# Kernel tuning notes

Measured on AMD Instinct MI355X. Metric: run time of the kernel, lower is better.

Reference implementation:

```python
import jax, jax.numpy as jnp
import numpy as np

B, N, C = 8, 8192, 512
H, DH = 8, C // 8
SCALE = 0.02


def setup_inputs() -> dict:
    key = jax.random.key(0)
    k0, k1, k2, k3, k4 = jax.random.split(key, 5)
    return {
        "x": jax.random.normal(k0, (B, N, C), dtype=jnp.float32),
        "w1": SCALE * jax.random.normal(k1, (2, H, DH, DH), dtype=jnp.float32),
        "b1": SCALE * jax.random.normal(k2, (2, H, DH), dtype=jnp.float32),
        "w2": SCALE * jax.random.normal(k3, (2, H, DH, DH), dtype=jnp.float32),
        "b2": SCALE * jax.random.normal(k4, (2, H, DH), dtype=jnp.float32),
    }


def reference(x, w1, b1, w2, b2):
    dtype = x.dtype
    x = x.astype(jnp.float32)
    b, n, c = x.shape
    xf = jnp.fft.rfft(x, axis=1, norm="ortho")            # [B, N//2+1, C] complex
    xf = xf.reshape(b, n // 2 + 1, H, DH)                  # [B, F, H, DH]
    xr, xi = jnp.real(xf), jnp.imag(xf)
    # per-head complex linear 1 + GELU (complex mult split into real/imag)
    o1r = jax.nn.gelu(
        jnp.einsum("bfhi,hio->bfho", xr, w1[0])
        - jnp.einsum("bfhi,hio->bfho", xi, w1[1]) + b1[0], approximate=False)
    o1i = jax.nn.gelu(
        jnp.einsum("bfhi,hio->bfho", xi, w1[0])
        + jnp.einsum("bfhi,hio->bfho", xr, w1[1]) + b1[1], approximate=False)
    # per-head complex linear 2
    o2r = (jnp.einsum("bfhi,hio->bfho", o1r, w2[0])
           - jnp.einsum("bfhi,hio->bfho", o1i, w2[1]) + b2[0])
    o2i = (jnp.einsum("bfhi,hio->bfho", o1i, w2[0])
           + jnp.einsum("bfhi,hio->bfho", o1r, w2[1]) + b2[1])
    yf = (o2r + 1j * o2i).reshape(b, n // 2 + 1, c)
    y = jnp.fft.irfft(yf, n=n, axis=1, norm="ortho")
    return y.astype(dtype)
```

## Files before the change

### kernel.cpp

```cpp
#include <hip/hip_runtime.h>
#include <math.h>

#define BB    8
#define NLEN  8192
#define CC    512
#define HH    8
#define DH    64
#define MH    4096
#define FREQ  4097
#define FP    4160
#define NSEQ  (BB*CC)
#define BHSZ  (65*4096)

#define KADDR(k) ((((k) >> 6) << 12) + ((k) & 63))

#define REGION_BYTES ((size_t)NSEQ * FP * 4ull)

static __device__ __align__(256) unsigned char g_scratch[2ull * (size_t)NSEQ * FP * 4ull];
__device__ unsigned short g_wprep[8 * 4 * 64 * 64];

typedef __attribute__((ext_vector_type(8))) short bf16x8;
typedef __attribute__((ext_vector_type(4))) float f32x4;
typedef __attribute__((ext_vector_type(4))) unsigned u32x4;

__device__ __forceinline__ f32x4 MFMA(bf16x8 a, bf16x8 b, f32x4 c){
  return __builtin_amdgcn_mfma_f32_16x16x32_bf16(a, b, c, 0, 0, 0);
}

__device__ __forceinline__ unsigned short f2bf(float f){
  unsigned u = __float_as_uint(f);
  return (unsigned short)((u + 0x7fffu + ((u >> 16) & 1u)) >> 16);
}
__device__ __forceinline__ unsigned pack2(float a, float b){
  return (unsigned)f2bf(a) | ((unsigned)f2bf(b) << 16);
}
__device__ __forceinline__ float bflo(unsigned u){ return __uint_as_float(u << 16); }
__device__ __forceinline__ float bfhi(unsigned u){ return __uint_as_float(u & 0xffff0000u); }

__device__ const float C32C[16] = {
  1.f, 0.98078528f, 0.92387953f, 0.83146961f, 0.70710678f, 0.55557023f,
  0.38268343f, 0.19509032f, 0.f, -0.19509032f, -0.38268343f, -0.55557023f,
  -0.70710678f, -0.83146961f, -0.92387953f, -0.98078528f};
__device__ const float C32S[16] = {
  0.f, 0.19509032f, 0.38268343f, 0.55557023f, 0.70710678f, 0.83146961f,
  0.92387953f, 0.98078528f, 1.f, 0.98078528f, 0.92387953f, 0.83146961f,
  0.70710678f, 0.55557023f, 0.38268343f, 0.19509032f};

__device__ __forceinline__ float gelu_fast(float v){
  float x  = v * 0.70710678118654752440f;
  float ax = fabsf(x);
  float t  = __builtin_amdgcn_rcpf(fmaf(0.3275911f, ax, 1.0f));
  float p  = fmaf(fmaf(fmaf(fmaf(1.061405429f, t, -1.453152027f), t,
                            1.421413741f), t, -0.284496736f), t, 0.254829592f);
  float e  = __expf(-x * x);
  float erf_ax = fmaf(-p * t, e, 1.0f);
  float erfx = copysignf(erf_ax, x);
  return 0.5f * v * (1.0f + erfx);
}

__device__ __forceinline__ float2 cadd(float2 a, float2 b){ return make_float2(a.x+b.x, a.y+b.y); }
__device__ __forceinline__ float2 csub(float2 a, float2 b){ return make_float2(a.x-b.x, a.y-b.y); }
__device__ __forceinline__ float2 cmul(float2 a, float2 b){
  return make_float2(fmaf(a.x, b.x, -(a.y*b.y)), fmaf(a.x, b.y, a.y*b.x));
}

__global__ __launch_bounds__(256) void transpose_in_k(const float* __restrict__ in,
                                                      unsigned* __restrict__ out){
  __shared__ float tile[64][33];
  int b  = blockIdx.z;
  int c0 = blockIdx.x * 32;
  int n0 = blockIdx.y * 64;
  int t  = threadIdx.x;
  int tx = t & 31, ty = t >> 5;
  const float* src = in + ((size_t)b * NLEN + n0) * CC + c0;
  #pragma unroll
  for (int k = 0; k < 8; ++k)
    tile[ty + 8*k][tx] = src[(size_t)(ty + 8*k) * CC + tx];
  __syncthreads();
  int lt = t & 15;
  int nl = 4 * lt;
  #pragma unroll
  for (int kk = 0; kk < 2; ++kk){
    int cl = (t >> 4) + 16*kk;
    uint2 u;
    u.x = pack2(tile[nl    ][cl], tile[nl + 1][cl]);
    u.y = pack2(tile[nl + 2][cl], tile[nl + 3][cl]);
    *(uint2*)(out + ((size_t)(b * CC + c0 + cl) * NLEN + n0) / 2 + 2*lt) = u;
  }
}

__global__ __launch_bounds__(256) void transpose_out_k(const unsigned* __restrict__ in,
                                                       float* __restrict__ out){
  __shared__ float tile[64][33];
  int b  = blockIdx.z;
  int c0 = blockIdx.x * 32;
  int n0 = blockIdx.y * 64;
  int t  = threadIdx.x;
  int lt = t & 15;
  int nl = 4 * lt;
  #pragma unroll
  for (int kk = 0; kk < 2; ++kk){
    int cl = (t >> 4) + 16*kk;
    uint2 u = *(const uint2*)(in + ((size_t)(b * CC + c0 + cl) * NLEN + n0) / 2 + 2*lt);
    tile[nl    ][cl] = bflo(u.x);
    tile[nl + 1][cl] = bfhi(u.x);
    tile[nl + 2][cl] = bflo(u.y);
    tile[nl + 3][cl] = bfhi(u.y);
  }
  __syncthreads();
  int tx = t & 31, ty = t >> 5;
  float* dst = out + ((size_t)b * NLEN + n0) * CC + c0;
  #pragma unroll
  for (int k = 0; k < 8; ++k)
    dst[(size_t)(ty + 8*k) * CC + tx] = tile[ty + 8*k][tx];
}

#define SL(e) ((e) + ((e) >> 4))
#define PERM16(p) ((((p) & 3) << 2) | ((p) >> 2))

template<int SIGN>
__device__ __forceinline__ void dft4ip(float2& v0, float2& v1, float2& v2, float2& v3){
  float2 s02 = cadd(v0, v2), d02 = csub(v0, v2);
  float2 s13 = cadd(v1, v3), d13 = csub(v1, v3);
  float2 id = make_float2(-(float)SIGN * d13.y, (float)SIGN * d13.x);
  v0 = cadd(s02, s13);
  v1 = cadd(d02, id);
  v2 = csub(s02, s13);
  v3 = csub(d02, id);
}

template<int SIGN>
__device__ __forceinline__ float2 w16c(int m){
  const float c1 = 0.9238795325112867f, s1 = 0.3826834323650898f, r = 0.7071067811865476f;
  float cs = 1.f, sn = 0.f;
  if (m == 1){ cs = c1;  sn = s1; }
  else if (m == 2){ cs = r;   sn = r; }
  else if (m == 3){ cs = s1;  sn = c1; }
  else if (m == 4){ cs = 0.f; sn = 1.f; }
  else if (m == 6){ cs = -r;  sn = r; }
  else if (m == 9){ cs = -c1; sn = -s1; }
  return make_float2(cs, (float)SIGN * sn);
}

template<int SIGN>
__device__ __forceinline__ void dft16ip(float2 v[16]){
  #pragma unroll
  for (int q0 = 0; q0 < 4; ++q0) dft4ip<SIGN>(v[q0], v[q0+4], v[q0+8], v[q0+12]);
  #pragma unroll
  for (int p0 = 0; p0 < 4; ++p0)
    #pragma unroll
    for (int q0 = 0; q0 < 4; ++q0){
      const int m = p0 * q0;
      if (m) v[q0 + 4*p0] = cmul(v[q0 + 4*p0], w16c<SIGN>(m));
    }
  #pragma unroll
  for (int p0 = 0; p0 < 4; ++p0) dft4ip<SIGN>(v[4*p0], v[4*p0+1], v[4*p0+2], v[4*p0+3]);
}

template<int SIGN>
__device__ __forceinline__ void twiddle16(float2 v[16], int jm, float invRNs){
  float ang = (float)SIGN * 6.2831853071795864769f * (float)jm * invRNs;
  float sn, cs; __sincosf(ang, &sn, &cs);
  float2 tw[16];
  tw[1] = make_float2(cs, sn);
  #pragma unroll
  for (int q = 2; q < 16; ++q) tw[q] = cmul(tw[q >> 1], tw[q - (q >> 1)]);
  #pragma unroll
  for (int q = 1; q < 16; ++q) v[q] = cmul(v[q], tw[q]);
}

template<int SIGN, int NS>
__device__ __forceinline__ void fft_mid_pass(float2* lds2, float2 v[16], int t){
  #pragma unroll
  for (int q = 0; q < 16; ++q) v[q] = lds2[SL(t + 256*q)];
  int jm = t & (NS - 1);
  if (NS > 1) twiddle16<SIGN>(v, jm, 1.0f / (16.0f * (float)NS));
  dft16ip<SIGN>(v);
  __syncthreads();
  int base = ((t - jm) << 4) + jm;
  #pragma unroll
  for (int p = 0; p < 16; ++p) lds2[SL(base + p*NS)] = v[PERM16(p)];
  __syncthreads();
}

#define ORTHO_S 0.011048543456039806f

__global__ __launch_bounds__(256) void fft_fwd_k(const unsigned* __restrict__ xt,
                                                 unsigned* __restrict__ spec){
  __shared__ float2 lds2[4352];
  int t = threadIdx.x;
  size_t row = blockIdx.x;
  const unsigned* src = xt + row * (NLEN/2);
  float2 v[16];
  #pragma unroll
  for (int q = 0; q < 16; ++q){
    unsigned u = src[t + 256*q];
    v[q] = make_float2(bflo(u), bfhi(u));
  }
  dft16ip<-1>(v);
  #pragma unroll
  for (int p = 0; p < 16; ++p) lds2[SL(16*t + p)] = v[PERM16(p)];
  __syncthreads();
  fft_mid_pass<-1, 16 >(lds2, v, t);
  fft_mid_pass<-1, 256>(lds2, v, t);
  unsigned* dst = spec + (row >> 6) * (size_t)BHSZ + (row & 63) * 64;
  float snb, csb;
  __sincosf(-6.2831853071795864769f * (float)t / (float)NLEN, &snb, &csb);
  #pragma unroll
  for (int q = 0; q < 8; ++q){
    int k = t + 256*q;
    float2 zk = lds2[SL(k)];
    float2 zc = lds2[SL((MH - k) & (MH - 1))];
    float ex = 0.5f*(zk.x + zc.x);
    float ey = 0.5f*(zk.y - zc.y);
    float ox =  0.5f*(zk.y + zc.y);
    float oy = -0.5f*(zk.x - zc.x);
    float cs = fmaf(csb, C32C[q],  snb*C32S[q]);
    float sn = fmaf(snb, C32C[q], -csb*C32S[q]);
    float P = cs*ox - sn*oy;
    float Q = cs*oy + sn*ox;
    dst[KADDR(k)]      = pack2(ORTHO_S*(ex + P), ORTHO_S*(ey + Q));
    dst[KADDR(MH - k)] = pack2(ORTHO_S*(ex - P), ORTHO_S*(Q - ey));
  }
  if (t == 0){
    float2 zm = lds2[SL(2048)];
    dst[KADDR(2048)] = pack2(ORTHO_S*zm.x, -ORTHO_S*zm.y);
  }
}

__global__ __launch_bounds__(256) void fft_inv_k(const unsigned* __restrict__ spec,
                                                 unsigned* __restrict__ yt){
  __shared__ float2 lds2[4352];
  int t = threadIdx.x;
  size_t row = blockIdx.x;
  const unsigned* src = spec + (row >> 6) * (size_t)BHSZ + (row & 63) * 64;
  float snb, csb;
  __sincosf(6.2831853071795864769f * (float)t / (float)NLEN, &snb, &csb);
  #pragma unroll
  for (int q = 0; q < 8; ++q){
    int k = t + 256*q;
    unsigned uk = src[KADDR(k)];
    unsigned uc = src[KADDR(MH - k)];
    float2 xk = make_float2(bflo(uk), bfhi(uk));
    float2 xc = make_float2(bflo(uc), bfhi(uc));
    if (k == 0){ xk.y = 0.0f; xc.y = 0.0f; }
    float ex = xk.x + xc.x;
    float ey = xk.y - xc.y;
    float dx = xk.x - xc.x;
    float dy = xk.y + xc.y;
    float cs = fmaf(csb, C32C[q], -snb*C32S[q]);
    float sn = fmaf(snb, C32C[q],  csb*C32S[q]);
    float ox = cs*dx - sn*dy;
    float oy = cs*dy + sn*dx;
    lds2[SL(k)] = make_float2(ex - oy, ey + ox);
    if (k > 0)
      lds2[SL(MH - k)] = make_float2(ex + oy, ox - ey);
  }
  if (t == 0){
    unsigned um = src[KADDR(2048)];
    lds2[SL(2048)] = make_float2(2.0f*bflo(um), -2.0f*bfhi(um));
  }
  __syncthreads();
  float2 v[16];
  fft_mid_pass<1, 1  >(lds2, v, t);
  fft_mid_pass<1, 16 >(lds2, v, t);
  fft_mid_pass<1, 256>(lds2, v, t);
  uint4* d4 = (uint4*)(yt + row * (NLEN/2) + 16*t);
  #pragma unroll
  for (int g = 0; g < 4; ++g){
    float2 w0 = lds2[SL(16*t + 4*g    )];
    float2 w1 = lds2[SL(16*t + 4*g + 1)];
    float2 w2 = lds2[SL(16*t + 4*g + 2)];
    float2 w3 = lds2[SL(16*t + 4*g + 3)];
    uint4 stv;
    stv.x = pack2(ORTHO_S*w0.x, ORTHO_S*w0.y);
    stv.y = pack2(ORTHO_S*w1.x, ORTHO_S*w1.y);
    stv.z = pack2(ORTHO_S*w2.x, ORTHO_S*w2.y);
    stv.w = pack2(ORTHO_S*w3.x, ORTHO_S*w3.y);
    d4[g] = stv;
  }
}

__global__ __launch_bounds__(256) void wprep_k(const float* __restrict__ w1,
                                               const float* __restrict__ w2){
  int t = threadIdx.x;
  int h = blockIdx.x;
  #pragma unroll 4
  for (int u = 0; u < 64; ++u){
    int idx = t + 256*u;
    int p = idx >> 12;
    int o = (idx >> 6) & 63;
    int jj = idx & 63;
    int swo = (o ^ (o >> 3)) & 7;
    int s = (((jj >> 3) ^ swo) << 3) | (jj & 7);
    int i;
    if (p < 2){
      i = s;
    } else {
      int ks = s >> 5, g = (s >> 3) & 3, j = s & 7;
      i = (2*ks + (j >> 2))*16 + 4*g + (j & 3);
    }
    const float* src = (p < 2) ? w1 : w2;
    float v = src[(size_t)(p & 1) * 32768 + (size_t)h * 4096 + i * 64 + o];
    g_wprep[(size_t)h * 16384 + idx] = f2bf(v);
  }
}

__global__ __launch_bounds__(256) void afno_mid_mfma_k(const unsigned* __restrict__ spec_in,
                                                       unsigned* __restrict__ spec_out,
                                                       const float* __restrict__ b1,
                                                       const float* __restrict__ b2){
  __shared__ unsigned short Wl[16384];
  const int t = threadIdx.x;
  const int bx = blockIdx.x, h = blockIdx.y, b = blockIdx.z;
  const size_t bhoff = (size_t)(b * HH + h) * BHSZ + (size_t)bx * 4096;
  const int l = t & 63, wv = t >> 6;
  const int lf = l & 15, lg = l >> 4;
  const int wf0 = wv * 16;

  const unsigned* xblk = spec_in + bhoff;
  unsigned bins[16];
  #pragma unroll
  for (int ks = 0; ks < 2; ++ks){
    int i0 = (ks*4 + lg) * 8;
    #pragma unroll
    for (int j = 0; j < 8; ++j)
      bins[ks*8 + j] = xblk[(i0 + j)*64 + wf0 + lf];
  }

  {
    const uint4* gw  = (const uint4*)(g_wprep + (size_t)h * 16384);
    uint4*       sw4 = (uint4*)Wl;
    #pragma unroll
    for (int u = 0; u < 8; ++u) sw4[t + 256*u] = gw[t + 256*u];
  }
  float4 br1[4], bi1[4];
  #pragma unroll
  for (int mt = 0; mt < 4; ++mt){
    br1[mt] = *(const float4*)(b1 +       (size_t)h*64 + mt*16 + lg*4);
    bi1[mt] = *(const float4*)(b1 + 512 + (size_t)h*64 + mt*16 + lg*4);
  }
  float b2r[4], b2i[4];
  #pragma unroll
  for (int nt = 0; nt < 4; ++nt){
    b2r[nt] = b2[(size_t)h*64 + nt*16 + lf];
    b2i[nt] = b2[512 + (size_t)h*64 + nt*16 + lf];
  }
  __syncthreads();

  const unsigned short* W1R = Wl;
  const unsigned short* W1I = Wl + 4096;
  const unsigned short* W2R = Wl + 8192;
  const unsigned short* W2I = Wl + 12288;
  const f32x4 zz = {0.f, 0.f, 0.f, 0.f};

  f32x4 a1R[4], a1I[4];
  #pragma unroll
  for (int mt = 0; mt < 4; ++mt){ a1R[mt] = zz; a1I[mt] = zz; }

  #pragma unroll
  for (int ks = 0; ks < 2; ++ks){
    u32x4 pr, pi;
    pr.x = __builtin_amdgcn_perm(bins[ks*8+1], bins[ks*8+0], 0x05040100u);
    pr.y = __builtin_amdgcn_perm(bins[ks*8+3], bins[ks*8+2], 0x05040100u);
    pr.z = __builtin_amdgcn_perm(bins[ks*8+5], bins[ks*8+4], 0x05040100u);
    pr.w = __builtin_amdgcn_perm(bins[ks*8+7], bins[ks*8+6], 0x05040100u);
    pi.x = __builtin_amdgcn_perm(bins[ks*8+1], bins[ks*8+0], 0x07060302u);
    pi.y = __builtin_amdgcn_perm(bins[ks*8+3], bins[ks*8+2], 0x07060302u);
    pi.z = __builtin_amdgcn_perm(bins[ks*8+5], bins[ks*8+4], 0x07060302u);
    pi.w = __builtin_amdgcn_perm(bins[ks*8+7], bins[ks*8+6], 0x07060302u);
    bf16x8 bxr = __builtin_bit_cast(bf16x8, pr);
    bf16x8 bxi = __builtin_bit_cast(bf16x8, pi);
    int b0 = ks*4 + lg;
    #pragma unroll
    for (int mt = 0; mt < 4; ++mt){
      int o = mt*16 + lf;
      int swo = (o ^ (o >> 3)) & 7;
      int off = o*64 + ((b0 ^ swo) << 3);
      bf16x8 awr  = *(const bf16x8*)(W1R + off);
      bf16x8 awi  = *(const bf16x8*)(W1I + off);
      bf16x8 awin = awi ^ (short)0x8000;
      a1R[mt] = MFMA(awr,  bxr, a1R[mt]);
      a1R[mt] = MFMA(awin, bxi, a1R[mt]);
      a1I[mt] = MFMA(awi,  bxr, a1I[mt]);
      a1I[mt] = MFMA(awr,  bxi, a1I[mt]);
    }
  }

  bf16x8 aFr[2], aFi[2], aFin[2];
  #pragma unroll
  for (int ks = 0; ks < 2; ++ks){
    const int m0 = 2*ks, m1 = 2*ks + 1;
    u32x4 wr4, wi4;
    wr4.x = pack2(gelu_fast(a1R[m0][0] + br1[m0].x), gelu_fast(a1R[m0][1] + br1[m0].y));
    wr4.y = pack2(gelu_fast(a1R[m0][2] + br1[m0].z), gelu_fast(a1R[m0][3] + br1[m0].w));
    wr4.z = pack2(gelu_fast(a1R[m1][0] + br1[m1].x), gelu_fast(a1R[m1][1] + br1[m1].y));
    wr4.w = pack2(gelu_fast(a1R[m1][2] + br1[m1].z), gelu_fast(a1R[m1][3] + br1[m1].w));
    wi4.x = pack2(gelu_fast(a1I[m0][0] + bi1[m0].x), gelu_fast(a1I[m0][1] + bi1[m0].y));
    wi4.y = pack2(gelu_fast(a1I[m0][2] + bi1[m0].z), gelu_fast(a1I[m0][3] + bi1[m0].w));
    wi4.z = pack2(gelu_fast(a1I[m1][0] + bi1[m1].x), gelu_fast(a1I[m1][1] + bi1[m1].y));
    wi4.w = pack2(gelu_fast(a1I[m1][2] + bi1[m1].z), gelu_fast(a1I[m1][3] + bi1[m1].w));
    aFr[ks]  = __builtin_bit_cast(bf16x8, wr4);
    aFi[ks]  = __builtin_bit_cast(bf16x8, wi4);
    aFin[ks] = aFi[ks] ^ (short)0x8000;
  }

  f32x4 a2R[4], a2I[4];
  #pragma unroll
  for (int nt = 0; nt < 4; ++nt){ a2R[nt] = zz; a2I[nt] = zz; }
  #pragma unroll
  for (int ks = 0; ks < 2; ++ks){
    int b0 = ks*4 + lg;
    #pragma unroll
    for (int nt = 0; nt < 4; ++nt){
      int o2 = nt*16 + lf;
      int swo = (o2 ^ (o2 >> 3)) & 7;
      int off = o2*64 + ((b0 ^ swo) << 3);
      bf16x8 bwr = *(const bf16x8*)(W2R + off);
      bf16x8 bwi = *(const bf16x8*)(W2I + off);
      a2R[nt] = MFMA(aFr[ks],  bwr, a2R[nt]);
      a2R[nt] = MFMA(aFin[ks], bwi, a2R[nt]);
      a2I[nt] = MFMA(aFi[ks],  bwr, a2I[nt]);
      a2I[nt] = MFMA(aFr[ks],  bwi, a2I[nt]);
    }
  }

  unsigned* oblk = spec_out + bhoff;
  int fl0 = wf0 + lg*4;
  #pragma unroll
  for (int nt = 0; nt < 4; ++nt){
    int o2 = nt*16 + lf;
    uint4 st;
    st.x = pack2(a2R[nt][0] + b2r[nt], a2I[nt][0] + b2i[nt]);
    st.y = pack2(a2R[nt][1] + b2r[nt], a2I[nt][1] + b2i[nt]);
    st.z = pack2(a2R[nt][2] + b2r[nt], a2I[nt][2] + b2i[nt]);
    st.w = pack2(a2R[nt][3] + b2r[nt], a2I[nt][3] + b2i[nt]);
    *(uint4*)(oblk + o2*64 + fl0) = st;
  }
}

extern "C" void kernel_launch(void* const* d_in, const int* in_sizes, int n_in,
                              void* d_out, int out_size, void* d_ws, size_t ws_size,
                              hipStream_t stream) {
  const float* x  = (const float*)d_in[0];
  const float* w1 = (const float*)d_in[1];
  const float* b1 = (const float*)d_in[2];
  const float* w2 = (const float*)d_in[3];
  const float* b2 = (const float*)d_in[4];
  float* out = (float*)d_out;

  unsigned char* base = (unsigned char*)d_ws;
  if (ws_size < 2 * REGION_BYTES){
    void* p = nullptr;
    hipGetSymbolAddress(&p, HIP_SYMBOL(g_scratch));
    base = (unsigned char*)p;
  }
  unsigned* specA = (unsigned*)base;
  unsigned char* regB = base + REGION_BYTES;
  unsigned* xt    = (unsigned*)regB;
  unsigned* specB = (unsigned*)regB;
  unsigned* ytp   = (unsigned*)base;

  wprep_k<<<8, 256, 0, stream>>>(w1, w2);
  transpose_in_k<<<dim3(CC/32, NLEN/64, BB), 256, 0, stream>>>(x, xt);
  fft_fwd_k<<<NSEQ, 256, 0, stream>>>(xt, specA);
  afno_mid_mfma_k<<<dim3(65, HH, BB), 256, 0, stream>>>(specA, specB, b1, b2);
  fft_inv_k<<<NSEQ, 256, 0, stream>>>(specB, ytp);
  transpose_out_k<<<dim3(CC/32, NLEN/64, BB), 256, 0, stream>>>(ytp, out);
}
```

Baseline: 205.5 us.

## Truncate bf16 packing, use sigmoid GELU approximation, pad LDS weight rows

Result: faster. 199.2 us (-3.1%).

```diff
diff --git a/kernel.cpp b/kernel.cpp
--- a/kernel.cpp
+++ b/kernel.cpp
@@ -34,6 +34,9 @@
 __device__ __forceinline__ unsigned pack2(float a, float b){
   return (unsigned)f2bf(a) | ((unsigned)f2bf(b) << 16);
 }
+__device__ __forceinline__ unsigned pack2t(float a, float b){
+  return __builtin_amdgcn_perm(__float_as_uint(b), __float_as_uint(a), 0x07060302u);
+}
 __device__ __forceinline__ float bflo(unsigned u){ return __uint_as_float(u << 16); }
 __device__ __forceinline__ float bfhi(unsigned u){ return __uint_as_float(u & 0xffff0000u); }
 
@@ -47,15 +50,8 @@
   0.70710678f, 0.55557023f, 0.38268343f, 0.19509032f};
 
 __device__ __forceinline__ float gelu_fast(float v){
-  float x  = v * 0.70710678118654752440f;
-  float ax = fabsf(x);
-  float t  = __builtin_amdgcn_rcpf(fmaf(0.3275911f, ax, 1.0f));
-  float p  = fmaf(fmaf(fmaf(fmaf(1.061405429f, t, -1.453152027f), t,
-                            1.421413741f), t, -0.284496736f), t, 0.254829592f);
-  float e  = __expf(-x * x);
-  float erf_ax = fmaf(-p * t, e, 1.0f);
-  float erfx = copysignf(erf_ax, x);
-  return 0.5f * v * (1.0f + erfx);
+  float e = __builtin_amdgcn_exp2f(-2.4554572f * v);
+  return v * __builtin_amdgcn_rcpf(1.0f + e);
 }
 
 __device__ __forceinline__ float2 cadd(float2 a, float2 b){ return make_float2(a.x+b.x, a.y+b.y); }
@@ -83,8 +79,8 @@
   for (int kk = 0; kk < 2; ++kk){
     int cl = (t >> 4) + 16*kk;
     uint2 u;
-    u.x = pack2(tile[nl    ][cl], tile[nl + 1][cl]);
-    u.y = pack2(tile[nl + 2][cl], tile[nl + 3][cl]);
+    u.x = pack2t(tile[nl    ][cl], tile[nl + 1][cl]);
+    u.y = pack2t(tile[nl + 2][cl], tile[nl + 3][cl]);
     *(uint2*)(out + ((size_t)(b * CC + c0 + cl) * NLEN + n0) / 2 + 2*lt) = u;
   }
 }
@@ -219,12 +215,12 @@
     float sn = fmaf(snb, C32C[q], -csb*C32S[q]);
     float P = cs*ox - sn*oy;
     float Q = cs*oy + sn*ox;
-    dst[KADDR(k)]      = pack2(ORTHO_S*(ex + P), ORTHO_S*(ey + Q));
-    dst[KADDR(MH - k)] = pack2(ORTHO_S*(ex - P), ORTHO_S*(Q - ey));
+    dst[KADDR(k)]      = pack2t(ORTHO_S*(ex + P), ORTHO_S*(ey + Q));
+    dst[KADDR(MH - k)] = pack2t(ORTHO_S*(ex - P), ORTHO_S*(Q - ey));
   }
   if (t == 0){
     float2 zm = lds2[SL(2048)];
-    dst[KADDR(2048)] = pack2(ORTHO_S*zm.x, -ORTHO_S*zm.y);
+    dst[KADDR(2048)] = pack2t(ORTHO_S*zm.x, -ORTHO_S*zm.y);
   }
 }
 
@@ -273,10 +269,10 @@
     float2 w2 = lds2[SL(16*t + 4*g + 2)];
     float2 w3 = lds2[SL(16*t + 4*g + 3)];
     uint4 stv;
-    stv.x = pack2(ORTHO_S*w0.x, ORTHO_S*w0.y);
-    stv.y = pack2(ORTHO_S*w1.x, ORTHO_S*w1.y);
-    stv.z = pack2(ORTHO_S*w2.x, ORTHO_S*w2.y);
-    stv.w = pack2(ORTHO_S*w3.x, ORTHO_S*w3.y);
+    stv.x = pack2t(ORTHO_S*w0.x, ORTHO_S*w0.y);
+    stv.y = pack2t(ORTHO_S*w1.x, ORTHO_S*w1.y);
+    stv.z = pack2t(ORTHO_S*w2.x, ORTHO_S*w2.y);
+    stv.w = pack2t(ORTHO_S*w3.x, ORTHO_S*w3.y);
     d4[g] = stv;
   }
 }
@@ -306,11 +302,13 @@
   }
 }
 
+#define WP 72
+#define WPLANE 4608
 __global__ __launch_bounds__(256) void afno_mid_mfma_k(const unsigned* __restrict__ spec_in,
                                                        unsigned* __restrict__ spec_out,
                                                        const float* __restrict__ b1,
                                                        const float* __restrict__ b2){
-  __shared__ unsigned short Wl[16384];
+  __shared__ unsigned short Wl[4 * WPLANE];
   const int t = threadIdx.x;
   const int bx = blockIdx.x, h = blockIdx.y, b = blockIdx.z;
   const size_t bhoff = (size_t)(b * HH + h) * BHSZ + (size_t)bx * 4096;
@@ -329,10 +327,13 @@
   }
 
   {
-    const uint4* gw  = (const uint4*)(g_wprep + (size_t)h * 16384);
-    uint4*       sw4 = (uint4*)Wl;
+    const uint4* gw = (const uint4*)(g_wprep + (size_t)h * 16384);
     #pragma unroll
-    for (int u = 0; u < 8; ++u) sw4[t + 256*u] = gw[t + 256*u];
+    for (int u = 0; u < 8; ++u){
+      int c = t + 256*u;
+      int p = c >> 9, o = (c >> 3) & 63, blk = c & 7;
+      *(uint4*)(Wl + p*WPLANE + o*WP + blk*8) = gw[c];
+    }
   }
   float4 br1[4], bi1[4];
   #pragma unroll
@@ -349,9 +350,9 @@
   __syncthreads();
 
   const unsigned short* W1R = Wl;
-  const unsigned short* W1I = Wl + 4096;
-  const unsigned short* W2R = Wl + 8192;
-  const unsigned short* W2I = Wl + 12288;
+  const unsigned short* W1I = Wl + WPLANE;
+  const unsigned short* W2R = Wl + 2*WPLANE;
+  const unsigned short* W2I = Wl + 3*WPLANE;
   const f32x4 zz = {0.f, 0.f, 0.f, 0.f};
 
   f32x4 a1R[4], a1I[4];
@@ -376,7 +377,7 @@
     for (int mt = 0; mt < 4; ++mt){
       int o = mt*16 + lf;
       int swo = (o ^ (o >> 3)) & 7;
-      int off = o*64 + ((b0 ^ swo) << 3);
+      int off = o*WP + ((b0 ^ swo) << 3);
       bf16x8 awr  = *(const bf16x8*)(W1R + off);
       bf16x8 awi  = *(const bf16x8*)(W1I + off);
       bf16x8 awin = awi ^ (short)0x8000;
@@ -392,14 +393,14 @@
   for (int ks = 0; ks < 2; ++ks){
     const int m0 = 2*ks, m1 = 2*ks + 1;
     u32x4 wr4, wi4;
-    wr4.x = pack2(gelu_fast(a1R[m0][0] + br1[m0].x), gelu_fast(a1R[m0][1] + br1[m0].y));
-    wr4.y = pack2(gelu_fast(a1R[m0][2] + br1[m0].z), gelu_fast(a1R[m0][3] + br1[m0].w));
-    wr4.z = pack2(gelu_fast(a1R[m1][0] + br1[m1].x), gelu_fast(a1R[m1][1] + br1[m1].y));
-    wr4.w = pack2(gelu_fast(a1R[m1][2] + br1[m1].z), gelu_fast(a1R[m1][3] + br1[m1].w));
-    wi4.x = pack2(gelu_fast(a1I[m0][0] + bi1[m0].x), gelu_fast(a1I[m0][1] + bi1[m0].y));
-    wi4.y = pack2(gelu_fast(a1I[m0][2] + bi1[m0].z), gelu_fast(a1I[m0][3] + bi1[m0].w));
-    wi4.z = pack2(gelu_fast(a1I[m1][0] + bi1[m1].x), gelu_fast(a1I[m1][1] + bi1[m1].y));
-    wi4.w = pack2(gelu_fast(a1I[m1][2] + bi1[m1].z), gelu_fast(a1I[m1][3] + bi1[m1].w));
+    wr4.x = pack2t(gelu_fast(a1R[m0][0] + br1[m0].x), gelu_fast(a1R[m0][1] + br1[m0].y));
+    wr4.y = pack2t(gelu_fast(a1R[m0][2] + br1[m0].z), gelu_fast(a1R[m0][3] + br1[m0].w));
+    wr4.z = pack2t(gelu_fast(a1R[m1][0] + br1[m1].x), gelu_fast(a1R[m1][1] + br1[m1].y));
+    wr4.w = pack2t(gelu_fast(a1R[m1][2] + br1[m1].z), gelu_fast(a1R[m1][3] + br1[m1].w));
+    wi4.x = pack2t(gelu_fast(a1I[m0][0] + bi1[m0].x), gelu_fast(a1I[m0][1] + bi1[m0].y));
+    wi4.y = pack2t(gelu_fast(a1I[m0][2] + bi1[m0].z), gelu_fast(a1I[m0][3] + bi1[m0].w));
+    wi4.z = pack2t(gelu_fast(a1I[m1][0] + bi1[m1].x), gelu_fast(a1I[m1][1] + bi1[m1].y));
+    wi4.w = pack2t(gelu_fast(a1I[m1][2] + bi1[m1].z), gelu_fast(a1I[m1][3] + bi1[m1].w));
     aFr[ks]  = __builtin_bit_cast(bf16x8, wr4);
     aFi[ks]  = __builtin_bit_cast(bf16x8, wi4);
     aFin[ks] = aFi[ks] ^ (short)0x8000;
@@ -415,7 +416,7 @@
     for (int nt = 0; nt < 4; ++nt){
       int o2 = nt*16 + lf;
       int swo = (o2 ^ (o2 >> 3)) & 7;
-      int off = o2*64 + ((b0 ^ swo) << 3);
+      int off = o2*WP + ((b0 ^ swo) << 3);
       bf16x8 bwr = *(const bf16x8*)(W2R + off);
       bf16x8 bwi = *(const bf16x8*)(W2I + off);
       a2R[nt] = MFMA(aFr[ks],  bwr, a2R[nt]);
@@ -431,10 +432,10 @@
   for (int nt = 0; nt < 4; ++nt){
     int o2 = nt*16 + lf;
     uint4 st;
-    st.x = pack2(a2R[nt][0] + b2r[nt], a2I[nt][0] + b2i[nt]);
-    st.y = pack2(a2R[nt][1] + b2r[nt], a2I[nt][1] + b2i[nt]);
-    st.z = pack2(a2R[nt][2] + b2r[nt], a2I[nt][2] + b2i[nt]);
-    st.w = pack2(a2R[nt][3] + b2r[nt], a2I[nt][3] + b2i[nt]);
+    st.x = pack2t(a2R[nt][0] + b2r[nt], a2I[nt][0] + b2i[nt]);
+    st.y = pack2t(a2R[nt][1] + b2r[nt], a2I[nt][1] + b2i[nt]);
+    st.z = pack2t(a2R[nt][2] + b2r[nt], a2I[nt][2] + b2i[nt]);
+    st.w = pack2t(a2R[nt][3] + b2r[nt], a2I[nt][3] + b2i[nt]);
     *(uint4*)(oblk + o2*64 + fl0) = st;
   }
 }
```
